# Performance work log

Measured on AMD Instinct MI355X. Metric: run time of the kernel, lower is better.

The kernel has to match this reference:

```python
import jax, jax.numpy as jnp
import numpy as np
from jax import lax

TAU = 0.05
N_ITERS = 4
TOPL = 64


def l2norm(x, axis):
    return x / (jnp.linalg.norm(x, axis=axis, keepdims=True) + 1e-6)


def setup_inputs() -> dict:
    key = jax.random.key(0)
    ks = jax.random.split(key, 8)
    B, N, Ck, Cv, H, W, L = 2, 4, 64, 512, 64, 64, 256
    qk = jax.random.normal(ks[0], (B, Ck, H, W), jnp.float32)
    qv = jax.random.normal(ks[1], (B, Cv, H, W), jnp.float32)
    qv_mem = jax.random.normal(ks[2], (B, N, Cv, H, W), jnp.float32)
    masks = jax.random.uniform(ks[3], (B, N, 2, H, W), jnp.float32)
    # random_init: normal(0, sqrt(2/L)) then l2norm over Ck (dim=-2)
    kappa0 = jax.random.normal(ks[4], (B, N, 2, Ck, L), jnp.float32) * np.sqrt(2.0 / L).astype(np.float32)
    kappa0 = l2norm(kappa0, axis=-2)
    nu0 = jnp.zeros((B, N, 2, Cv, L), jnp.float32)
    zita0 = jnp.full((B, N, 2, 1, L), 1e-6, jnp.float32)
    Cin = 2 * Cv + 2 * TOPL  # 1152
    Wf = jax.random.normal(ks[5], (Cv, Cin, 3, 3), jnp.float32) * 0.02
    bf = jnp.zeros((Cv,), jnp.float32)
    Wa = jax.random.normal(ks[6], (Cv, Cin, 3, 3), jnp.float32) * 0.02
    ba = jnp.zeros((Cv,), jnp.float32)
    return {"qk": qk, "qv": qv, "qv_mem": qv_mem, "masks": masks,
            "kappa0": kappa0, "nu0": nu0, "zita0": zita0,
            "Wf": Wf, "bf": bf, "Wa": Wa, "ba": ba}


def reference(qk, qv, qv_mem, masks, kappa0, nu0, zita0, Wf, bf, Wa, ba):
    B, Ck, H, W = qk.shape
    N = masks.shape[1]
    Cv = qv.shape[1]
    L = kappa0.shape[-1]
    HW = H * W

    # ---- swem: EM iterations (torch runs these under no_grad) ----
    x = qk.reshape(B, 1, 1, Ck, HW)            # (B,1,1,Ck,HW)
    m = masks.reshape(B, N, 2, HW, 1)          # (B,N,2,HW,1)
    x_t = jnp.swapaxes(x, -2, -1)              # (B,1,1,HW,Ck)
    x_t_n = l2norm(x_t, axis=-1)

    weights = m
    kappa = kappa0
    z = None
    zita = None
    for i in range(N_ITERS):
        # swe_step: softmax((z - max)/tau) == softmax(z/tau), stable
        kn = l2norm(kappa, axis=-2)
        zz = jnp.matmul(x_t, kn)               # (B,N,2,HW,L)
        zz = jax.nn.softmax(zz / TAU, axis=-1) * weights
        # swm_step
        zita = zita0 + zz.sum(axis=-2, keepdims=True)            # (B,N,2,1,L)
        kappa = (zita0 * kappa0 + jnp.matmul(x, zz)) / zita      # (B,N,2,Ck,L)
        z = zz
        if i < N_ITERS - 1:
            # sww_step
            kn = l2norm(kappa, axis=-2)
            s = jnp.matmul(x_t_n, kn)                            # (B,N,2,HW,L)
            mx = jnp.max(s, axis=-1, keepdims=True)
            mx = jnp.max(mx, axis=2, keepdims=True)
            s_exp = jnp.exp((s - mx) / TAU)
            sum_exp = s_exp.sum(axis=-1, keepdims=True)          # (B,N,2,HW,1)
            props = sum_exp / sum_exp.sum(axis=2, keepdims=True)
            weights = m * (1.0 - props)

    mv_flat = qv_mem.reshape(B, N, 1, Cv, HW)                    # (B,N,1,Cv,HW)
    nu = (zita0 * nu0 + jnp.matmul(mv_flat, z)) / zita           # (B,N,2,Cv,L)

    # ---- matching / get_affinity ----
    qk_n = l2norm(qk, axis=1)
    mk = l2norm(kappa, axis=-2)
    qk_ = qk_n.reshape(B, 1, 1, Ck, HW)
    aff = jnp.matmul(jnp.swapaxes(mk, -2, -1), qk_)              # (B,N,2,L,HW)
    mx = jnp.max(aff, axis=2, keepdims=True)
    mx = jnp.max(mx, axis=3, keepdims=True)
    exp_aff = jnp.exp((aff - mx) / TAU)
    p_aff = exp_aff / exp_aff.sum(axis=(2, 3), keepdims=True)
    p_aff = p_aff.reshape(B, N, 2 * L, HW)

    # ---- perm_inv_feat: top-l over L, cumulative sums (vectorized) ----
    ea = exp_aff.reshape(B * N, 2, L, H, W)
    sorted_aff = lax.top_k(jnp.moveaxis(ea, 2, -1), TOPL)[0]     # (BN,2,H,W,TOPL) desc
    feat = jnp.cumsum(sorted_aff, axis=-1)
    Sf = feat[:, 0] / (feat[:, 0] + feat[:, 1])                  # (BN,H,W,TOPL)
    Sf = jnp.moveaxis(Sf, -1, 1)                                 # (BN,TOPL,H,W)
    S = jnp.concatenate([Sf, 1.0 - Sf], axis=1)                  # (BN,2*TOPL,H,W)

    # ---- memory readout ----
    mv2 = jnp.swapaxes(nu, 2, 3).reshape(B, N, Cv, 2 * L)
    mem_out = jnp.matmul(mv2, p_aff).reshape(B * N, Cv, H, W)

    qv_e = jnp.broadcast_to(qv[:, None], (B, N, Cv, H, W)).reshape(B * N, Cv, H, W)
    fin = jnp.concatenate([mem_out, qv_e, S], axis=1)            # (BN, 2*Cv+2*TOPL, H, W)

    # ---- FeatureFusionLayer: gated 3x3 convs ----
    dn = ('NCHW', 'OIHW', 'NCHW')
    f = lax.conv_general_dilated(fin, Wf, (1, 1), 'SAME', dimension_numbers=dn) + bf[None, :, None, None]
    a = lax.conv_general_dilated(fin, Wa, (1, 1), 'SAME', dimension_numbers=dn) + ba[None, :, None, None]
    return f * jax.nn.sigmoid(a)
```

## Files before the change

### kernel.cpp

```cpp
#include <hip/hip_runtime.h>
#include <hip/hip_bf16.h>
#include <math.h>


typedef __attribute__((ext_vector_type(8))) short bf16x8;
typedef __attribute__((ext_vector_type(4))) float f32x4;
typedef __attribute__((ext_vector_type(16))) float f32x16;

static __device__ __forceinline__ short f2b(float f){
  __hip_bfloat16 h = __float2bfloat16(f);
  short s; __builtin_memcpy(&s, &h, 2); return s;
}
static __device__ __forceinline__ unsigned pack2(float lo, float hi){
  return (unsigned)(unsigned short)f2b(lo) | ((unsigned)(unsigned short)f2b(hi) << 16);
}

static __device__ __forceinline__ float wred_max(float v){
  #pragma unroll
  for (int off = 32; off > 0; off >>= 1) v = fmaxf(v, __shfl_xor(v, off));
  return v;
}
static __device__ __forceinline__ float wred_sum(float v){
  #pragma unroll
  for (int off = 32; off > 0; off >>= 1) v += __shfl_xor(v, off);
  return v;
}

static __device__ __forceinline__ void gload_lds16(const short* g, short* l){
  __builtin_amdgcn_global_load_lds((const __attribute__((address_space(1))) unsigned int*)(g),
                                   (__attribute__((address_space(3))) unsigned int*)(l),
                                   16, 0, 0);
}

#define FMA16(X0,X1,X2,X3,KV) \
  acc[0]+=X0.x*KV; acc[1]+=X0.y*KV; acc[2]+=X0.z*KV; acc[3]+=X0.w*KV; \
  acc[4]+=X1.x*KV; acc[5]+=X1.y*KV; acc[6]+=X1.z*KV; acc[7]+=X1.w*KV; \
  acc[8]+=X2.x*KV; acc[9]+=X2.y*KV; acc[10]+=X2.z*KV; acc[11]+=X2.w*KV; \
  acc[12]+=X3.x*KV; acc[13]+=X3.y*KV; acc[14]+=X3.z*KV; acc[15]+=X3.w*KV;


__global__ void k_prep_x(const float* __restrict__ qk, float* __restrict__ xT, float* __restrict__ xTn){
  int idx = blockIdx.x*256 + threadIdx.x;
  int b = idx >> 12, hw = idx & 4095;
  float v[64]; float ss = 0.f;
  #pragma unroll
  for (int k=0;k<64;k++){ v[k] = qk[((size_t)b*64 + k)*4096 + hw]; ss += v[k]*v[k]; }
  float inv = 1.f/(sqrtf(ss) + 1e-6f);
  #pragma unroll
  for (int k=0;k<64;k++){ xT[(size_t)idx*64 + k] = v[k]; xTn[(size_t)idx*64 + k] = v[k]*inv; }
}

__global__ void k_init_w_kn(const float* __restrict__ masks, const float* __restrict__ kappa0,
                            float* __restrict__ wts, float* __restrict__ kn){
  int t = blockIdx.x*256 + threadIdx.x;
  if (t < 16*4096) wts[t] = masks[t];
  if (t < 16*256){
    int bng = t >> 8, l = t & 255;
    float ss = 0.f;
    #pragma unroll 4
    for (int k=0;k<64;k++){ float v = kappa0[((size_t)bng*64 + k)*256 + l]; ss += v*v; }
    float inv = 1.f/(sqrtf(ss) + 1e-6f);
    #pragma unroll 4
    for (int k=0;k<64;k++) kn[((size_t)bng*64 + k)*256 + l] = kappa0[((size_t)bng*64 + k)*256 + l]*inv;
  }
}

__global__ void k_prep_wt2(const float* __restrict__ Wsrc, short* __restrict__ Wt2, int conv){
  int t = blockIdx.x*256 + threadIdx.x;
  int j = t & 7;
  int cvl = (t >> 3) & 63;
  int kh = (t >> 9) & 1;
  int rest = t >> 10;
  int r = rest % 9;
  int tile = rest / 9;
  int cb = tile % 72;
  int cvb = tile / 72;
  int cv = cvb*64 + cvl;
  int cin = cb*16 + kh*8 + j;
  Wt2[((size_t)tile*2 + conv)*9216 + (r*2 + kh)*512 + cvl*8 + j] = f2b(Wsrc[((size_t)cv*1152 + cin)*9 + r]);
}

__global__ void k_qv_fin(const float* __restrict__ qv, unsigned* __restrict__ fin32){
  int t = blockIdx.x*256 + threadIdx.x;
  int bn = t >> 20;
  int rem = t & 1048575;
  int p = rem >> 12;
  int hw = rem & 4095;
  int b = bn >> 2;
  float lo = qv[((size_t)b*512 + 2*p)*4096 + hw];
  float hi = qv[((size_t)b*512 + 2*p + 1)*4096 + hw];
  fin32[(size_t)bn*2359296 + (size_t)(256 + p)*4096 + hw] = pack2(lo, hi);
}


__global__ __launch_bounds__(256) void k_zz(const float* __restrict__ xT, const float* __restrict__ kn,
                                            const float* __restrict__ wts, float* __restrict__ zzb){
  int blk = blockIdx.x;
  int bng = blk >> 8;
  int hw0 = (blk & 255) * 16;
  int b = bng >> 3;
  int t = threadIdx.x;
  int lane = t & 63, wid = t >> 6;
  __shared__ float xs[64][16];
  __shared__ float redm[4], reds[4];
  {
    int k = t & 63, pq = t >> 6;
    #pragma unroll
    for (int p = pq; p < 16; p += 4)
      xs[k][p] = xT[((size_t)b*4096 + hw0 + p)*64 + k];
  }
  float acc[16];
  #pragma unroll
  for (int p=0;p<16;p++) acc[p] = 0.f;
  __syncthreads();
  const float* knp = kn + (size_t)bng*16384 + t;
  #pragma unroll 2
  for (int k=0;k<64;k++){
    float knv = knp[k*256];
    float4 x0 = *(const float4*)&xs[k][0];
    float4 x1 = *(const float4*)&xs[k][4];
    float4 x2 = *(const float4*)&xs[k][8];
    float4 x3 = *(const float4*)&xs[k][12];
    FMA16(x0,x1,x2,x3,knv)
  }
  #pragma unroll
  for (int p=0;p<16;p++){
    float v = acc[p];
    float m = wred_max(v);
    if (lane==0) redm[wid] = m;
    __syncthreads();
    m = fmaxf(fmaxf(redm[0],redm[1]), fmaxf(redm[2],redm[3]));
    float e = __expf((v - m) * 20.0f);
    float s = wred_sum(e);
    if (lane==0) reds[wid] = s;
    __syncthreads();
    s = reds[0]+reds[1]+reds[2]+reds[3];
    float wgt = wts[bng*4096 + hw0 + p];
    zzb[((size_t)bng*4096 + hw0 + p)*256 + t] = e/s*wgt;
  }
}

__global__ __launch_bounds__(1024) void k_part(const float* __restrict__ qk, const float* __restrict__ zzb,
                                               float* __restrict__ kpart, float* __restrict__ zpart){
  int bng = blockIdx.x >> 4, ch = blockIdx.x & 15;
  int b = bng >> 3;
  int t = threadIdx.x; int l = t & 255; int kq = t >> 8;
  __shared__ float xs[64][80];
  float acc[16];
  #pragma unroll
  for (int j=0;j<16;j++) acc[j]=0.f;
  float zs = 0.f;
  for (int sc=0; sc<4; sc++){
    int hwb = ch*256 + sc*64;
    __syncthreads();
    {
      int hw_l = t & 63, kk = t >> 6;
      #pragma unroll
      for (int k = kk; k < 64; k += 16)
        xs[hw_l][k] = qk[((size_t)b*64 + k)*4096 + hwb + hw_l];
    }
    __syncthreads();
    #pragma unroll 2
    for (int hw_l=0; hw_l<64; hw_l++){
      float zv = zzb[((size_t)bng*4096 + hwb + hw_l)*256 + l];
      zs += zv;
      const float* xp = &xs[hw_l][kq*16];
      float4 x0 = *(const float4*)(xp);
      float4 x1 = *(const float4*)(xp+4);
      float4 x2 = *(const float4*)(xp+8);
      float4 x3 = *(const float4*)(xp+12);
      FMA16(x0,x1,x2,x3,zv)
    }
  }
  #pragma unroll
  for (int j=0;j<16;j++)
    kpart[(((size_t)bng*16 + ch)*64 + kq*16 + j)*256 + l] = acc[j];
  if (kq == 0) zpart[((size_t)bng*16 + ch)*256 + l] = zs;
}

__global__ __launch_bounds__(1024) void k_fin(const float* __restrict__ kpart, const float* __restrict__ zpart,
                                              const float* __restrict__ kappa0, const float* __restrict__ zita0,
                                              float* __restrict__ kn, float* __restrict__ zita){
  int bng = blockIdx.x; int t = threadIdx.x; int l = t & 255; int kq = t >> 8;
  float z0 = zita0[bng*256 + l];
  float zs = z0;
  #pragma unroll
  for (int ch=0; ch<16; ch++) zs += zpart[((size_t)bng*16 + ch)*256 + l];
  if (kq==0) zita[bng*256 + l] = zs;
  float inv = 1.f/zs;
  float kap[16]; float ss = 0.f;
  #pragma unroll
  for (int j=0;j<16;j++){
    int k = kq*16 + j;
    float a = z0 * kappa0[((size_t)bng*64 + k)*256 + l];
    #pragma unroll
    for (int ch=0; ch<16; ch++) a += kpart[(((size_t)bng*16 + ch)*64 + k)*256 + l];
    float kv = a*inv; kap[j] = kv; ss += kv*kv;
  }
  __shared__ float ssr[4][256];
  ssr[kq][l] = ss;
  __syncthreads();
  float tot = ssr[0][l]+ssr[1][l]+ssr[2][l]+ssr[3][l];
  float ninv = 1.f/(sqrtf(tot) + 1e-6f);
  #pragma unroll
  for (int j=0;j<16;j++) kn[((size_t)bng*64 + kq*16 + j)*256 + l] = kap[j]*ninv;
}

__global__ __launch_bounds__(512) void k_sww(const float* __restrict__ xTn, const float* __restrict__ kn,
                                             const float* __restrict__ masks, float* __restrict__ wts){
  int blk = blockIdx.x;
  int bnI = blk >> 8;
  int hw0 = (blk & 255)*16;
  int b = bnI >> 2;
  int t = threadIdx.x;
  int lane = t & 63, wid = t >> 6;
  int g = t >> 8; int l = t & 255;
  int bng = bnI*2 + g;
  __shared__ float xs[64][16];
  __shared__ float redm[8], reds[8];
  {
    int k = t & 63, pq = t >> 6;
    #pragma unroll
    for (int p = pq; p < 16; p += 8)
      xs[k][p] = xTn[((size_t)b*4096 + hw0 + p)*64 + k];
  }
  float knr[64];
  const float* knp = kn + (size_t)bng*16384 + l;
  #pragma unroll
  for (int k=0;k<64;k++) knr[k] = knp[k*256];
  float acc[16];
  #pragma unroll
  for (int p=0;p<16;p++) acc[p]=0.f;
  __syncthreads();
  #pragma unroll 2
  for (int k=0;k<64;k++){
    float knv = knr[k];
    float4 x0 = *(const float4*)&xs[k][0];
    float4 x1 = *(const float4*)&xs[k][4];
    float4 x2 = *(const float4*)&xs[k][8];
    float4 x3 = *(const float4*)&xs[k][12];
    FMA16(x0,x1,x2,x3,knv)
  }
  #pragma unroll
  for (int p=0;p<16;p++){
    float v = acc[p];
    float m = wred_max(v);
    if (lane==0) redm[wid] = m;
    __syncthreads();
    m = fmaxf(fmaxf(fmaxf(redm[0],redm[1]),fmaxf(redm[2],redm[3])),
              fmaxf(fmaxf(redm[4],redm[5]),fmaxf(redm[6],redm[7])));
    float e = __expf((v - m) * 20.0f);
    float s = wred_sum(e);
    if (lane==0) reds[wid] = s;
    __syncthreads();
    float s0 = reds[0]+reds[1]+reds[2]+reds[3];
    float s1 = reds[4]+reds[5]+reds[6]+reds[7];
    if (lane==0 && (wid==0 || wid==4)){
      float sg = g ? s1 : s0;
      wts[bng*4096 + hw0 + p] = masks[bng*4096 + hw0 + p]*(1.f - sg/(s0+s1));
    }
  }
}

__global__ __launch_bounds__(512) void k_aff(const float* __restrict__ xTn, const float* __restrict__ kn,
                                             float* __restrict__ paff){
  int blk = blockIdx.x;
  int bnI = blk >> 8;
  int hw0 = (blk & 255)*16;
  int b = bnI >> 2;
  int t = threadIdx.x;
  int lane = t & 63, wid = t >> 6;
  int g = t >> 8; int l = t & 255;
  int bng = bnI*2 + g;
  __shared__ float xs[64][16];
  __shared__ float redm[8], reds[8];
  {
    int k = t & 63, pq = t >> 6;
    #pragma unroll
    for (int p = pq; p < 16; p += 8)
      xs[k][p] = xTn[((size_t)b*4096 + hw0 + p)*64 + k];
  }
  float knr[64];
  const float* knp = kn + (size_t)bng*16384 + l;
  #pragma unroll
  for (int k=0;k<64;k++) knr[k] = knp[k*256];
  float acc[16];
  #pragma unroll
  for (int p=0;p<16;p++) acc[p]=0.f;
  __syncthreads();
  #pragma unroll 2
  for (int k=0;k<64;k++){
    float knv = knr[k];
    float4 x0 = *(const float4*)&xs[k][0];
    float4 x1 = *(const float4*)&xs[k][4];
    float4 x2 = *(const float4*)&xs[k][8];
    float4 x3 = *(const float4*)&xs[k][12];
    FMA16(x0,x1,x2,x3,knv)
  }
  #pragma unroll
  for (int p=0;p<16;p++){
    float v = acc[p];
    float m = wred_max(v);
    if (lane==0) redm[wid] = m;
    __syncthreads();
    m = fmaxf(fmaxf(fmaxf(redm[0],redm[1]),fmaxf(redm[2],redm[3])),
              fmaxf(fmaxf(redm[4],redm[5]),fmaxf(redm[6],redm[7])));
    float e = __expf((v - m) * 20.0f);
    float s = wred_sum(e);
    if (lane==0) reds[wid] = s;
    __syncthreads();
    float tot = reds[0]+reds[1]+reds[2]+reds[3]+reds[4]+reds[5]+reds[6]+reds[7];
    paff[((size_t)bnI*4096 + hw0 + p)*512 + t] = e/tot;
  }
}


static __device__ __forceinline__ float topk_cum(float va, float vb, float vc, float vd, int lane){
  float run = 0.f, cme = 0.f;
  #pragma unroll 2
  for (int tt=0; tt<64; tt++){
    float m = fmaxf(fmaxf(va,vb), fmaxf(vc,vd));
    float wm = wred_max(m);
    run += wm;
    if (lane == tt) cme = run;
    unsigned long long ball = __ballot(m == wm);
    int wl = __ffsll(ball) - 1;
    if (lane == wl){
      if (va == wm) va = -1.f;
      else if (vb == wm) vb = -1.f;
      else if (vc == wm) vc = -1.f;
      else vd = -1.f;
    }
  }
  return cme;
}

__global__ __launch_bounds__(256) void k_topk(const float* __restrict__ paff, unsigned* __restrict__ fin32){
  int wid = threadIdx.x >> 6, lane = threadIdx.x & 63;
  int px = blockIdx.x*4 + wid;
  int bn = px >> 12, hw = px & 4095;
  const float* row = paff + (size_t)px*512;
  float4 a0 = *(const float4*)(row + lane*4);
  float4 a1 = *(const float4*)(row + 256 + lane*4);
  float c0 = topk_cum(a0.x,a0.y,a0.z,a0.w, lane);
  float c1 = topk_cum(a1.x,a1.y,a1.z,a1.w, lane);
  float sf = c0/(c0+c1);
  float sf2 = __shfl_down(sf, 1);
  if (!(lane & 1)){
    size_t base = (size_t)bn*2359296;
    fin32[base + (size_t)(512 + (lane>>1))*4096 + hw] = pack2(sf, sf2);
    fin32[base + (size_t)(544 + (lane>>1))*4096 + hw] = pack2(1.f - sf, 1.f - sf2);
  }
}


__global__ __launch_bounds__(256) void k_nu(const float* __restrict__ qvm, const float* __restrict__ zzb,
                                            const float* __restrict__ nu0, const float* __restrict__ zita0,
                                            const float* __restrict__ zita, short* __restrict__ mv2){
  constexpr int AP = 40;
  __shared__ short lA[64*AP];
  __shared__ short lB[64*AP];
  int blk = blockIdx.x;
  int bng = blk >> 5, cvb = (blk >> 2) & 7, lb = blk & 3;
  int bn = bng >> 1, g = bng & 1;
  int t = threadIdx.x, lane = t & 63, w = t >> 6;
  int wm = w >> 1, wn = w & 1;
  int quad = lane >> 4, fr = lane & 15;
  f32x4 acc[2][2] = {};
  const float* Ab = qvm + ((size_t)bn*512 + cvb*64)*4096;
  const float* Bb = zzb + (size_t)bng*4096*256 + lb*64;
  int arow = t >> 2, acg = (t & 3)*8;
  int bhw = t & 31, blg = (t >> 5)*8;
  for (int k0 = 0; k0 < 4096; k0 += 32){
    __syncthreads();
    {
      const float* s = Ab + (size_t)arow*4096 + k0 + acg;
      float4 f0 = *(const float4*)s, f1 = *(const float4*)(s+4);
      bf16x8 v;
      v[0]=f2b(f0.x); v[1]=f2b(f0.y); v[2]=f2b(f0.z); v[3]=f2b(f0.w);
      v[4]=f2b(f1.x); v[5]=f2b(f1.y); v[6]=f2b(f1.z); v[7]=f2b(f1.w);
      *(bf16x8*)&lA[arow*AP + acg] = v;
    }
    {
      const float* s = Bb + (size_t)(k0 + bhw)*256 + blg;
      float4 f0 = *(const float4*)s, f1 = *(const float4*)(s+4);
      lB[(blg+0)*AP + bhw] = f2b(f0.x);
      lB[(blg+1)*AP + bhw] = f2b(f0.y);
      lB[(blg+2)*AP + bhw] = f2b(f0.z);
      lB[(blg+3)*AP + bhw] = f2b(f0.w);
      lB[(blg+4)*AP + bhw] = f2b(f1.x);
      lB[(blg+5)*AP + bhw] = f2b(f1.y);
      lB[(blg+6)*AP + bhw] = f2b(f1.z);
      lB[(blg+7)*AP + bhw] = f2b(f1.w);
    }
    __syncthreads();
    int koff = quad*8;
    bf16x8 a0 = *(const bf16x8*)&lA[(wm*32 +  0 + fr)*AP + koff];
    bf16x8 a1 = *(const bf16x8*)&lA[(wm*32 + 16 + fr)*AP + koff];
    bf16x8 b0 = *(const bf16x8*)&lB[(wn*32 +  0 + fr)*AP + koff];
    bf16x8 b1 = *(const bf16x8*)&lB[(wn*32 + 16 + fr)*AP + koff];
    acc[0][0] = __builtin_amdgcn_mfma_f32_16x16x32_bf16(a0,b0,acc[0][0],0,0,0);
    acc[0][1] = __builtin_amdgcn_mfma_f32_16x16x32_bf16(a0,b1,acc[0][1],0,0,0);
    acc[1][0] = __builtin_amdgcn_mfma_f32_16x16x32_bf16(a1,b0,acc[1][0],0,0,0);
    acc[1][1] = __builtin_amdgcn_mfma_f32_16x16x32_bf16(a1,b1,acc[1][1],0,0,0);
  }
  #pragma unroll
  for (int mf=0; mf<2; mf++)
  #pragma unroll
  for (int nf=0; nf<2; nf++)
  #pragma unroll
  for (int r=0;r<4;r++){
    int cv = cvb*64 + wm*32 + mf*16 + quad*4 + r;
    int l  = lb*64 + wn*32 + nf*16 + fr;
    float c = acc[mf][nf][r];
    float z0 = zita0[bng*256 + l];
    float nv = (z0 * nu0[((size_t)bng*512 + cv)*256 + l] + c) / zita[bng*256 + l];
    mv2[((size_t)bn*512 + cv)*512 + g*256 + l] = f2b(nv);
  }
}

__global__ __launch_bounds__(256) void k_mem(const short* __restrict__ mv2, const float* __restrict__ paff,
                                             unsigned* __restrict__ fin32){
  constexpr int BP = 40;
  __shared__ short lB[256*BP];
  int blk = blockIdx.x;
  int bn = blk >> 7, cvb = (blk >> 4) & 7, hwb = blk & 15;
  int t = threadIdx.x, lane = t & 63, w = t >> 6;
  int quad = lane >> 4, fr = lane & 15;
  f32x4 acc[4][4] = {};
  const short* Ab = mv2 + ((size_t)bn*512 + cvb*64)*512;
  const float* Bb = paff + ((size_t)bn*4096 + hwb*256)*512;
  for (int k0=0; k0<512; k0+=32){
    __syncthreads();
    {
      const float* s = Bb + (size_t)t*512 + k0;
      #pragma unroll
      for (int q=0;q<4;q++){
        float4 f0 = *(const float4*)(s + q*8);
        float4 f1 = *(const float4*)(s + q*8 + 4);
        bf16x8 v;
        v[0]=f2b(f0.x); v[1]=f2b(f0.y); v[2]=f2b(f0.z); v[3]=f2b(f0.w);
        v[4]=f2b(f1.x); v[5]=f2b(f1.y); v[6]=f2b(f1.z); v[7]=f2b(f1.w);
        *(bf16x8*)&lB[t*BP + q*8] = v;
      }
    }
    __syncthreads();
    int koff = quad*8;
    bf16x8 af[4];
    #pragma unroll
    for (int mf=0; mf<4; mf++)
      af[mf] = *(const bf16x8*)(Ab + (size_t)(mf*16 + fr)*512 + k0 + koff);
    #pragma unroll
    for (int nf=0; nf<4; nf++){
      bf16x8 bv = *(const bf16x8*)&lB[(w*64 + nf*16 + fr)*BP + koff];
      #pragma unroll
      for (int mf=0; mf<4; mf++)
        acc[mf][nf] = __builtin_amdgcn_mfma_f32_16x16x32_bf16(af[mf], bv, acc[mf][nf],0,0,0);
    }
  }
  #pragma unroll
  for (int mf=0;mf<4;mf++)
  #pragma unroll
  for (int nf=0;nf<4;nf++){
    int hw = hwb*256 + w*64 + nf*16 + fr;
    int p0 = cvb*32 + mf*8 + quad*2;
    unsigned lo = pack2(acc[mf][nf][0], acc[mf][nf][1]);
    unsigned hi = pack2(acc[mf][nf][2], acc[mf][nf][3]);
    fin32[(size_t)bn*2359296 + (size_t)p0*4096 + hw] = lo;
    fin32[(size_t)bn*2359296 + (size_t)(p0+1)*4096 + hw] = hi;
  }
}

__global__ __launch_bounds__(256, 2) void k_conv(const unsigned* __restrict__ fin32,
                                                 const short* __restrict__ Wt2,
                                                 const float* __restrict__ bfv, const float* __restrict__ bav,
                                                 float* __restrict__ out){
  __shared__ __attribute__((aligned(16))) unsigned lFu[2][2*6*66*4];
  __shared__ __attribute__((aligned(16))) short wbuf[2*9216];
  int blk = blockIdx.x;
  int bn = blk >> 7, cvb = (blk >> 4) & 7, yb = blk & 15;
  int t = threadIdx.x, lane = t & 63, wv = t >> 6;
  int ln = lane & 31, kh = lane >> 5;
  int y0 = yb*4;
  f32x16 accF[2][2] = {}, accA[2][2] = {};
  const unsigned* finB = fin32 + (size_t)bn*2359296;
  const short* Wslice = Wt2 + (size_t)cvb*72*18432;
  if (t < 192){
    int pj = t & 3; int side = (t >> 2) & 1; int row = (t >> 3) % 6; int khz = (t / 48) & 1; int buf = t / 96;
    lFu[buf][((khz*6 + row)*66 + (side ? 65 : 0))*4 + pj] = 0u;
  }
  int tks[3], tkh[3], tgy[3];
  #pragma unroll
  for (int i = 0; i < 3; i++){
    int tk = wv*3 + i;
    tkh[i] = (tk >= 6) ? 1 : 0;
    tks[i] = tk - tkh[i]*6;
    tgy[i] = y0 - 1 + tks[i];
  }
  unsigned stg[3][4];

#define LOAD_STG(CB) { \
    _Pragma("unroll") \
    for (int i = 0; i < 3; i++){ \
      bool ok = (tgy[i] >= 0 && tgy[i] < 64); \
      _Pragma("unroll") \
      for (int pj = 0; pj < 4; pj++) \
        stg[i][pj] = ok ? finB[(size_t)((CB)*8 + tkh[i]*4 + pj)*4096 + tgy[i]*64 + lane] : 0u; \
    } }
#define WRITE_STG(BUF) { \
    _Pragma("unroll") \
    for (int i = 0; i < 3; i++){ \
      uint4 v; v.x = stg[i][0]; v.y = stg[i][1]; v.z = stg[i][2]; v.w = stg[i][3]; \
      *(uint4*)&lFu[BUF][((tkh[i]*6 + tks[i])*66 + lane + 1)*4] = v; \
    } }
#define DMA_H0(CB) { \
    const short* src = Wslice + (size_t)(CB)*18432 + lane*8; \
    _Pragma("unroll") \
    for (int j = 0; j < 5; j++){ \
      int i = wv*5 + j; \
      int idx = (i < 10) ? i : i + 8; \
      gload_lds16(src + idx*512, &wbuf[idx*512]); \
    } }
#define DMA_H1(CB) { \
    const short* src = Wslice + (size_t)(CB)*18432 + lane*8; \
    _Pragma("unroll") \
    for (int j = 0; j < 4; j++){ \
      int i = wv*4 + j; \
      int idx = (i < 8) ? i + 10 : i + 20; \
      gload_lds16(src + idx*512, &wbuf[idx*512]); \
    } }
#define CONV_COMPUTE(R9LO, R9HI, BUF) { \
    _Pragma("unroll") \
    for (int r9 = (R9LO); r9 < (R9HI); r9++){ \
      int dy = r9/3, dx = r9 - dy*3; \
      bf16x8 f0 = *(const bf16x8*)(wbuf + r9*1024 + kh*512 + ln*8); \
      bf16x8 f1 = *(const bf16x8*)(wbuf + r9*1024 + kh*512 + ln*8 + 256); \
      bf16x8 a0 = *(const bf16x8*)(wbuf + 9216 + r9*1024 + kh*512 + ln*8); \
      bf16x8 a1 = *(const bf16x8*)(wbuf + 9216 + r9*1024 + kh*512 + ln*8 + 256); \
      int row = wv + dy; \
      _Pragma("unroll") \
      for (int xh = 0; xh < 2; xh++){ \
        bf16x8 bv = *(const bf16x8*)((const short*)&lFu[BUF][0] + (((kh*6 + row)*66 + xh*32 + ln + dx)*8)); \
        accF[0][xh] = __builtin_amdgcn_mfma_f32_32x32x16_bf16(f0, bv, accF[0][xh],0,0,0); \
        accF[1][xh] = __builtin_amdgcn_mfma_f32_32x32x16_bf16(f1, bv, accF[1][xh],0,0,0); \
        accA[0][xh] = __builtin_amdgcn_mfma_f32_32x32x16_bf16(a0, bv, accA[0][xh],0,0,0); \
        accA[1][xh] = __builtin_amdgcn_mfma_f32_32x32x16_bf16(a1, bv, accA[1][xh],0,0,0); \
      } \
    } }

  LOAD_STG(0)
  WRITE_STG(0)
  DMA_H0(0)
  int cur = 0;
  for (int cb = 0; cb < 72; cb++){
    __syncthreads();
    DMA_H1(cb)
    CONV_COMPUTE(0, 5, cur)
    __syncthreads();
    int nx = (cb < 71) ? cb + 1 : 71;
    LOAD_STG(nx)
    if (cb < 71) DMA_H0(cb + 1)
    CONV_COMPUTE(5, 9, cur)
    WRITE_STG(cur ^ 1)
    cur ^= 1;
  }
#undef LOAD_STG
#undef WRITE_STG
#undef DMA_H0
#undef DMA_H1
#undef CONV_COMPUTE
  int y = y0 + wv;
  #pragma unroll
  for (int mf = 0; mf < 2; mf++)
  #pragma unroll
  for (int xh = 0; xh < 2; xh++){
    int x = xh*32 + ln;
    #pragma unroll
    for (int reg = 0; reg < 16; reg++){
      int cv = cvb*64 + mf*32 + 4*kh + 8*(reg>>2) + (reg&3);
      float fv = accF[mf][xh][reg] + bfv[cv];
      float av = accA[mf][xh][reg] + bav[cv];
      out[((size_t)bn*512 + cv)*4096 + (size_t)y*64 + x] = fv/(1.f + __expf(-av));
    }
  }
}


extern "C" void kernel_launch(void* const* d_in, const int* in_sizes, int n_in,
                              void* d_out, int out_size, void* d_ws, size_t ws_size,
                              hipStream_t stream){
  const float* qk     = (const float*)d_in[0];
  const float* qv     = (const float*)d_in[1];
  const float* qvm    = (const float*)d_in[2];
  const float* masks  = (const float*)d_in[3];
  const float* kappa0 = (const float*)d_in[4];
  const float* nu0    = (const float*)d_in[5];
  const float* zita0  = (const float*)d_in[6];
  const float* Wf     = (const float*)d_in[7];
  const float* bfb    = (const float*)d_in[8];
  const float* Wa     = (const float*)d_in[9];
  const float* bab    = (const float*)d_in[10];
  float* out = (float*)d_out;

  float* ws    = (float*)d_ws;
  float* zzb   = ws;
  float* kpart = zzb + 16777216;
  float* zpart = kpart + 4194304;
  float* kn    = zpart + 65536;
  float* zita  = kn + 262144;
  float* wts   = zita + 4096;
  float* xT    = wts + 65536;
  float* xTn   = xT + 524288;
  short* mv2   = (short*)(xTn + 524288);
  unsigned* fin32 = (unsigned*)(mv2 + 4194304);
  short* Wt2   = (short*)(fin32 + 18874368);

  k_prep_x<<<32, 256, 0, stream>>>(qk, xT, xTn);
  k_init_w_kn<<<256, 256, 0, stream>>>(masks, kappa0, wts, kn);
  k_prep_wt2<<<20736, 256, 0, stream>>>(Wf, Wt2, 0);
  k_prep_wt2<<<20736, 256, 0, stream>>>(Wa, Wt2, 1);
  k_qv_fin<<<32768, 256, 0, stream>>>(qv, fin32);

  for (int it = 0; it < 4; ++it){
    k_zz<<<4096, 256, 0, stream>>>(xT, kn, wts, zzb);
    k_part<<<256, 1024, 0, stream>>>(qk, zzb, kpart, zpart);
    k_fin<<<16, 1024, 0, stream>>>(kpart, zpart, kappa0, zita0, kn, zita);
    if (it < 3) k_sww<<<2048, 512, 0, stream>>>(xTn, kn, masks, wts);
  }

  k_nu<<<512, 256, 0, stream>>>(qvm, zzb, nu0, zita0, zita, mv2);
  k_aff<<<2048, 512, 0, stream>>>(xTn, kn, zzb );
  k_topk<<<8192, 256, 0, stream>>>(zzb, fin32);
  k_mem<<<1024, 256, 0, stream>>>(mv2, zzb, fin32);
  k_conv<<<1024, 256, 0, stream>>>(fin32, Wt2, bfb, bab, out);
}
```

Before: 2.367 ms.

## Compute shared qv conv contribution once per batch instead of per memory slot

```diff
diff --git a/kernel.cpp b/kernel.cpp
--- a/kernel.cpp
+++ b/kernel.cpp
@@ -471,11 +471,109 @@
   }
 }
 
+
+#define CONV_STAGE_DECL \
+  unsigned stg[3][4];
+#define CONV_LOAD_STG(CB) { \
+    _Pragma("unroll") \
+    for (int i = 0; i < 3; i++){ \
+      int tk = wv*3 + i; \
+      int skh = (tk >= 6) ? 1 : 0; \
+      int srow = tk - skh*6; \
+      int gy = y0 - 1 + srow; \
+      bool ok = (gy >= 0 && gy < 64); \
+      _Pragma("unroll") \
+      for (int pj = 0; pj < 4; pj++) \
+        stg[i][pj] = ok ? finB[(size_t)((CB)*8 + skh*4 + pj)*4096 + gy*64 + lane] : 0u; \
+    } }
+#define CONV_WRITE_STG { \
+    _Pragma("unroll") \
+    for (int i = 0; i < 3; i++){ \
+      int tk = wv*3 + i; \
+      int skh = (tk >= 6) ? 1 : 0; \
+      int srow = tk - skh*6; \
+      uint4 v; v.x = stg[i][0]; v.y = stg[i][1]; v.z = stg[i][2]; v.w = stg[i][3]; \
+      *(uint4*)&lFu[((skh*6 + srow)*66 + lane + 1)*4] = v; \
+    } }
+#define CONV_DMA_W(CB) { \
+    const short* src = Wslice + (size_t)(CB)*18432 + lane*8; \
+    _Pragma("unroll") \
+    for (int i = 0; i < 9; i++){ \
+      int idx = wv*9 + i; \
+      gload_lds16(src + idx*512, &wbuf[idx*512]); \
+    } }
+#define CONV_COMPUTE { \
+    __builtin_amdgcn_s_setprio(1); \
+    _Pragma("unroll 3") \
+    for (int r9 = 0; r9 < 9; r9++){ \
+      int dy = r9/3, dx = r9 - dy*3; \
+      bf16x8 f0 = *(const bf16x8*)(wbuf + r9*1024 + kh*512 + ln*8); \
+      bf16x8 f1 = *(const bf16x8*)(wbuf + r9*1024 + kh*512 + ln*8 + 256); \
+      bf16x8 a0 = *(const bf16x8*)(wbuf + 9216 + r9*1024 + kh*512 + ln*8); \
+      bf16x8 a1 = *(const bf16x8*)(wbuf + 9216 + r9*1024 + kh*512 + ln*8 + 256); \
+      int row = wv + dy; \
+      _Pragma("unroll") \
+      for (int xh = 0; xh < 2; xh++){ \
+        bf16x8 bv = *(const bf16x8*)((const short*)lFu + (((kh*6 + row)*66 + xh*32 + ln + dx)*8)); \
+        accF[0][xh] = __builtin_amdgcn_mfma_f32_32x32x16_bf16(f0, bv, accF[0][xh],0,0,0); \
+        accF[1][xh] = __builtin_amdgcn_mfma_f32_32x32x16_bf16(f1, bv, accF[1][xh],0,0,0); \
+        accA[0][xh] = __builtin_amdgcn_mfma_f32_32x32x16_bf16(a0, bv, accA[0][xh],0,0,0); \
+        accA[1][xh] = __builtin_amdgcn_mfma_f32_32x32x16_bf16(a1, bv, accA[1][xh],0,0,0); \
+      } \
+    } \
+    __builtin_amdgcn_s_setprio(0); }
+#define CONV_HALO_ZERO \
+  if (t < 96){ \
+    int pj = t & 3; int side = (t >> 2) & 1; int row = (t >> 3) % 6; int khz = t / 48; \
+    lFu[((khz*6 + row)*66 + (side ? 65 : 0))*4 + pj] = 0u; \
+  }
+
+__global__ __launch_bounds__(256, 2) void k_convu(const unsigned* __restrict__ fin32,
+                                                  const short* __restrict__ Wt2,
+                                                  float* __restrict__ U){
+  __shared__ __attribute__((aligned(16))) unsigned lFu[2*6*66*4];
+  __shared__ __attribute__((aligned(16))) short wbuf[2*9216];
+  int blk = blockIdx.x;
+  int h = blk >> 8, b = (blk >> 7) & 1, cvb = (blk >> 4) & 7, yb = blk & 15;
+  int t = threadIdx.x, lane = t & 63, wv = t >> 6;
+  int ln = lane & 31, kh = lane >> 5;
+  int y0 = yb*4;
+  f32x16 accF[2][2] = {}, accA[2][2] = {};
+  const unsigned* finB = fin32 + (size_t)(b*4)*2359296;
+  const short* Wslice = Wt2 + (size_t)cvb*72*18432;
+  CONV_HALO_ZERO
+  CONV_STAGE_DECL
+  for (int i = 0; i < 16; i++){
+    int cb = 32 + h*16 + i;
+    CONV_LOAD_STG(cb)
+    __syncthreads();
+    CONV_WRITE_STG
+    CONV_DMA_W(cb)
+    __syncthreads();
+    CONV_COMPUTE
+  }
+  int y = y0 + wv;
+  #pragma unroll
+  for (int mf = 0; mf < 2; mf++)
+  #pragma unroll
+  for (int xh = 0; xh < 2; xh++){
+    int x = xh*32 + ln;
+    #pragma unroll
+    for (int reg = 0; reg < 16; reg++){
+      int cv = cvb*64 + mf*32 + 4*kh + 8*(reg>>2) + (reg&3);
+      size_t o = (size_t)cv*4096 + (size_t)y*64 + x;
+      U[((size_t)(h*2 + 0)*2 + b)*2097152 + o] = accF[mf][xh][reg];
+      U[((size_t)(h*2 + 1)*2 + b)*2097152 + o] = accA[mf][xh][reg];
+    }
+  }
+}
+
 __global__ __launch_bounds__(256, 2) void k_conv(const unsigned* __restrict__ fin32,
                                                  const short* __restrict__ Wt2,
                                                  const float* __restrict__ bfv, const float* __restrict__ bav,
+                                                 const float* __restrict__ U,
                                                  float* __restrict__ out){
-  __shared__ __attribute__((aligned(16))) unsigned lFu[2][2*6*66*4];
+  __shared__ __attribute__((aligned(16))) unsigned lFu[2*6*66*4];
   __shared__ __attribute__((aligned(16))) short wbuf[2*9216];
   int blk = blockIdx.x;
   int bn = blk >> 7, cvb = (blk >> 4) & 7, yb = blk & 15;
@@ -485,91 +583,19 @@
   f32x16 accF[2][2] = {}, accA[2][2] = {};
   const unsigned* finB = fin32 + (size_t)bn*2359296;
   const short* Wslice = Wt2 + (size_t)cvb*72*18432;
-  if (t < 192){
-    int pj = t & 3; int side = (t >> 2) & 1; int row = (t >> 3) % 6; int khz = (t / 48) & 1; int buf = t / 96;
-    lFu[buf][((khz*6 + row)*66 + (side ? 65 : 0))*4 + pj] = 0u;
-  }
-  int tks[3], tkh[3], tgy[3];
-  #pragma unroll
-  for (int i = 0; i < 3; i++){
-    int tk = wv*3 + i;
-    tkh[i] = (tk >= 6) ? 1 : 0;
-    tks[i] = tk - tkh[i]*6;
-    tgy[i] = y0 - 1 + tks[i];
-  }
-  unsigned stg[3][4];
-
-#define LOAD_STG(CB) { \
-    _Pragma("unroll") \
-    for (int i = 0; i < 3; i++){ \
-      bool ok = (tgy[i] >= 0 && tgy[i] < 64); \
-      _Pragma("unroll") \
-      for (int pj = 0; pj < 4; pj++) \
-        stg[i][pj] = ok ? finB[(size_t)((CB)*8 + tkh[i]*4 + pj)*4096 + tgy[i]*64 + lane] : 0u; \
-    } }
-#define WRITE_STG(BUF) { \
-    _Pragma("unroll") \
-    for (int i = 0; i < 3; i++){ \
-      uint4 v; v.x = stg[i][0]; v.y = stg[i][1]; v.z = stg[i][2]; v.w = stg[i][3]; \
-      *(uint4*)&lFu[BUF][((tkh[i]*6 + tks[i])*66 + lane + 1)*4] = v; \
-    } }
-#define DMA_H0(CB) { \
-    const short* src = Wslice + (size_t)(CB)*18432 + lane*8; \
-    _Pragma("unroll") \
-    for (int j = 0; j < 5; j++){ \
-      int i = wv*5 + j; \
-      int idx = (i < 10) ? i : i + 8; \
-      gload_lds16(src + idx*512, &wbuf[idx*512]); \
-    } }
-#define DMA_H1(CB) { \
-    const short* src = Wslice + (size_t)(CB)*18432 + lane*8; \
-    _Pragma("unroll") \
-    for (int j = 0; j < 4; j++){ \
-      int i = wv*4 + j; \
-      int idx = (i < 8) ? i + 10 : i + 20; \
-      gload_lds16(src + idx*512, &wbuf[idx*512]); \
-    } }
-#define CONV_COMPUTE(R9LO, R9HI, BUF) { \
-    _Pragma("unroll") \
-    for (int r9 = (R9LO); r9 < (R9HI); r9++){ \
-      int dy = r9/3, dx = r9 - dy*3; \
-      bf16x8 f0 = *(const bf16x8*)(wbuf + r9*1024 + kh*512 + ln*8); \
-      bf16x8 f1 = *(const bf16x8*)(wbuf + r9*1024 + kh*512 + ln*8 + 256); \
-      bf16x8 a0 = *(const bf16x8*)(wbuf + 9216 + r9*1024 + kh*512 + ln*8); \
-      bf16x8 a1 = *(const bf16x8*)(wbuf + 9216 + r9*1024 + kh*512 + ln*8 + 256); \
-      int row = wv + dy; \
-      _Pragma("unroll") \
-      for (int xh = 0; xh < 2; xh++){ \
-        bf16x8 bv = *(const bf16x8*)((const short*)&lFu[BUF][0] + (((kh*6 + row)*66 + xh*32 + ln + dx)*8)); \
-        accF[0][xh] = __builtin_amdgcn_mfma_f32_32x32x16_bf16(f0, bv, accF[0][xh],0,0,0); \
-        accF[1][xh] = __builtin_amdgcn_mfma_f32_32x32x16_bf16(f1, bv, accF[1][xh],0,0,0); \
-        accA[0][xh] = __builtin_amdgcn_mfma_f32_32x32x16_bf16(a0, bv, accA[0][xh],0,0,0); \
-        accA[1][xh] = __builtin_amdgcn_mfma_f32_32x32x16_bf16(a1, bv, accA[1][xh],0,0,0); \
-      } \
-    } }
-
-  LOAD_STG(0)
-  WRITE_STG(0)
-  DMA_H0(0)
-  int cur = 0;
-  for (int cb = 0; cb < 72; cb++){
-    __syncthreads();
-    DMA_H1(cb)
-    CONV_COMPUTE(0, 5, cur)
-    __syncthreads();
-    int nx = (cb < 71) ? cb + 1 : 71;
-    LOAD_STG(nx)
-    if (cb < 71) DMA_H0(cb + 1)
-    CONV_COMPUTE(5, 9, cur)
-    WRITE_STG(cur ^ 1)
-    cur ^= 1;
-  }
-#undef LOAD_STG
-#undef WRITE_STG
-#undef DMA_H0
-#undef DMA_H1
-#undef CONV_COMPUTE
+  CONV_HALO_ZERO
+  CONV_STAGE_DECL
+  for (int i = 0; i < 40; i++){
+    int cb = (i < 32) ? i : i + 32;
+    CONV_LOAD_STG(cb)
+    __syncthreads();
+    CONV_WRITE_STG
+    CONV_DMA_W(cb)
+    __syncthreads();
+    CONV_COMPUTE
+  }
   int y = y0 + wv;
+  int b = bn >> 2;
   #pragma unroll
   for (int mf = 0; mf < 2; mf++)
   #pragma unroll
@@ -578,8 +604,11 @@
     #pragma unroll
     for (int reg = 0; reg < 16; reg++){
       int cv = cvb*64 + mf*32 + 4*kh + 8*(reg>>2) + (reg&3);
-      float fv = accF[mf][xh][reg] + bfv[cv];
-      float av = accA[mf][xh][reg] + bav[cv];
+      size_t o = (size_t)cv*4096 + (size_t)y*64 + x;
+      float fv = accF[mf][xh][reg] + bfv[cv]
+               + U[((size_t)0*2 + b)*2097152 + o] + U[((size_t)2*2 + b)*2097152 + o];
+      float av = accA[mf][xh][reg] + bav[cv]
+               + U[((size_t)1*2 + b)*2097152 + o] + U[((size_t)3*2 + b)*2097152 + o];
       out[((size_t)bn*512 + cv)*4096 + (size_t)y*64 + x] = fv/(1.f + __expf(-av));
     }
   }
@@ -614,6 +643,7 @@
   short* mv2   = (short*)(xTn + 524288);
   unsigned* fin32 = (unsigned*)(mv2 + 4194304);
   short* Wt2   = (short*)(fin32 + 18874368);
+  float* U     = zzb;
 
   k_prep_x<<<32, 256, 0, stream>>>(qk, xT, xTn);
   k_init_w_kn<<<256, 256, 0, stream>>>(masks, kappa0, wts, kn);
@@ -632,5 +662,6 @@
   k_aff<<<2048, 512, 0, stream>>>(xTn, kn, zzb );
   k_topk<<<8192, 256, 0, stream>>>(zzb, fin32);
   k_mem<<<1024, 256, 0, stream>>>(mv2, zzb, fin32);
-  k_conv<<<1024, 256, 0, stream>>>(fin32, Wt2, bfb, bab, out);
-}
+  k_convu<<<512, 256, 0, stream>>>(fin32, Wt2, U);
+  k_conv<<<1024, 256, 0, stream>>>(fin32, Wt2, bfb, bab, U, out);
+}
```

Result: faster. 2.220 ms (-6.2%).
